# Kernel optimization log

Hardware: AMD Instinct MI355X
Metric: run time of the kernel (lower is better)

Reference implementation:

```python
import jax, jax.numpy as jnp
import numpy as np

EPS = 1e-5

def _layernorm(x, g, b):
    mu = jnp.mean(x, axis=-1, keepdims=True)
    var = jnp.mean(jnp.square(x - mu), axis=-1, keepdims=True)
    return (x - mu) * jax.lax.rsqrt(var + EPS) * g + b

def _time_shift(x):
    # xx[:, t] = x[:, t-1], xx[:, 0] = 0  (ZeroPad2d((0,0,1,-1)))
    return jnp.pad(x, ((0, 0), (1, 0), (0, 0)))[:, :-1, :]

def _wkv(time_decay, time_first, k, v):
    # Numerically-stable RWKV v4 recurrence (matches wkv_cuda forward).
    # k, v: [B, T, C]; time_decay, time_first: [C]
    w = -jnp.exp(time_decay)  # negative decay
    u = time_first
    B, T, C = k.shape
    aa0 = jnp.zeros((B, C), k.dtype)
    bb0 = jnp.zeros((B, C), k.dtype)
    pp0 = jnp.full((B, C), -1e38, k.dtype)

    def step(carry, kv_t):
        aa, bb, pp = carry
        kt, vt = kv_t
        ww = u + kt
        p = jnp.maximum(pp, ww)
        e1 = jnp.exp(pp - p)
        e2 = jnp.exp(ww - p)
        yt = (e1 * aa + e2 * vt) / (e1 * bb + e2)
        ww2 = pp + w
        p2 = jnp.maximum(ww2, kt)
        e1b = jnp.exp(ww2 - p2)
        e2b = jnp.exp(kt - p2)
        return (e1b * aa + e2b * vt, e1b * bb + e2b, p2), yt

    kT = jnp.swapaxes(k, 0, 1)  # [T, B, C]
    vT = jnp.swapaxes(v, 0, 1)
    _, y = jax.lax.scan(step, (aa0, bb0, pp0), (kT, vT))
    return jnp.swapaxes(y, 0, 1)  # [B, T, C]


def setup_inputs() -> dict:
    num_layers, layer_id, C = 8, 1, 512
    B, T = 512, 50
    H = 4 * C
    key = jax.random.key(0)
    ks = jax.random.split(key, 12)

    # parameter init mirroring the torch module's structured init
    ratio_0_to_1 = layer_id / (num_layers - 1)
    ratio_1_to_almost0 = 1.0 - layer_id / num_layers
    h = np.arange(C, dtype=np.float32)
    time_decay = (-5 + 8 * (h / (C - 1)) ** (0.7 + 1.3 * ratio_0_to_1)).astype(np.float32)
    zigzag = (np.array([(i + 1) % 3 - 1 for i in range(C)], dtype=np.float32)) * 0.5
    time_first = (np.ones(C, dtype=np.float32) * np.log(0.3) + zigzag).astype(np.float32)
    xr = (h / C).astype(np.float32)
    att_mix_k = (xr ** ratio_1_to_almost0)[None, None, :].astype(np.float32)
    att_mix_v = (xr ** ratio_1_to_almost0 + 0.3 * ratio_0_to_1)[None, None, :].astype(np.float32)
    att_mix_r = (xr ** (0.5 * ratio_1_to_almost0))[None, None, :].astype(np.float32)
    ffn_mix_k = att_mix_k.copy()
    ffn_mix_r = att_mix_k.copy()

    s = 0.02
    return {
        "x": jax.random.normal(ks[0], (B, T, C), jnp.float32),
        "ln1_g": jnp.ones((C,), jnp.float32), "ln1_b": jnp.zeros((C,), jnp.float32),
        "ln2_g": jnp.ones((C,), jnp.float32), "ln2_b": jnp.zeros((C,), jnp.float32),
        "att_mix_k": jnp.asarray(att_mix_k), "att_mix_v": jnp.asarray(att_mix_v),
        "att_mix_r": jnp.asarray(att_mix_r),
        "time_decay": jnp.asarray(time_decay), "time_first": jnp.asarray(time_first),
        "Wk": jax.random.normal(ks[1], (C, C), jnp.float32) * s,
        "Wv": jax.random.normal(ks[2], (C, C), jnp.float32) * s,
        "Wr": jax.random.normal(ks[3], (C, C), jnp.float32) * s,
        "Wo": jax.random.normal(ks[4], (C, C), jnp.float32) * s,
        "ffn_mix_k": jnp.asarray(ffn_mix_k), "ffn_mix_r": jnp.asarray(ffn_mix_r),
        "Fk": jax.random.normal(ks[5], (H, C), jnp.float32) * s,
        "Fv": jax.random.normal(ks[6], (C, H), jnp.float32) * s,
        "Fr": jax.random.normal(ks[7], (C, C), jnp.float32) * s,
    }


def reference(x, ln1_g, ln1_b, ln2_g, ln2_b,
              att_mix_k, att_mix_v, att_mix_r, time_decay, time_first,
              Wk, Wv, Wr, Wo, ffn_mix_k, ffn_mix_r, Fk, Fv, Fr):
    # --- time-mix (attention) branch ---
    h = _layernorm(x, ln1_g, ln1_b)
    hh = _time_shift(h)
    xk = h * att_mix_k + hh * (1 - att_mix_k)
    xv = h * att_mix_v + hh * (1 - att_mix_v)
    xr = h * att_mix_r + hh * (1 - att_mix_r)
    k = jnp.einsum('btc,dc->btd', xk, Wk)
    v = jnp.einsum('btc,dc->btd', xv, Wv)
    sr = jax.nn.sigmoid(jnp.einsum('btc,dc->btd', xr, Wr))
    rwkv = sr * _wkv(time_decay, time_first, k, v)
    x = x + jnp.einsum('btc,dc->btd', rwkv, Wo)

    # --- channel-mix (FFN) branch ---
    h = _layernorm(x, ln2_g, ln2_b)
    hh = _time_shift(h)
    fk = h * ffn_mix_k + hh * (1 - ffn_mix_k)
    fr = h * ffn_mix_r + hh * (1 - ffn_mix_r)
    kk = jnp.einsum('btc,hc->bth', fk, Fk)
    kk = jnp.square(jax.nn.relu(kk))
    kv = jnp.einsum('bth,ch->btc', kk, Fv)
    rkv = jax.nn.sigmoid(jnp.einsum('btc,dc->btd', fr, Fr)) * kv
    return x + rkv
```

## Files before the change

### kernel.cpp

```cpp
#include <hip/hip_runtime.h>
#include <stdint.h>

typedef unsigned short u16;
typedef __bf16 bf16x8 __attribute__((ext_vector_type(8)));
typedef float f32x4 __attribute__((ext_vector_type(4)));

#define DEV static __device__ __forceinline__

DEV u16 f2b(float f) {
    unsigned u = __float_as_uint(f);
    u += 0x7FFF + ((u >> 16) & 1);
    return (u16)(u >> 16);
}
DEV float b2f(u16 h) { return __uint_as_float((unsigned)h << 16); }

DEV void load16(const void* g, void* l) {
    __builtin_amdgcn_global_load_lds((const __attribute__((address_space(1))) void*)g,
                                     (__attribute__((address_space(3))) void*)l, 16, 0, 0);
}

__global__ __launch_bounds__(256) void cvt_bf16(const float* __restrict__ src,
                                                u16* __restrict__ dst, int n) {
    int i = (blockIdx.x * 256 + threadIdx.x) * 4;
    if (i < n) {
        float4 f = *(const float4*)(src + i);
        ushort4 o;
        o.x = f2b(f.x); o.y = f2b(f.y); o.z = f2b(f.z); o.w = f2b(f.w);
        *(ushort4*)(dst + i) = o;
    }
}

template <int NOUT>
__global__ __launch_bounds__(256) void ln_mix(
    const float* __restrict__ x, const float* __restrict__ g, const float* __restrict__ be,
    const float* __restrict__ mk, const float* __restrict__ mv, const float* __restrict__ mr,
    u16* __restrict__ ok, u16* __restrict__ ov, u16* __restrict__ orr, int T) {
    const int C = 512;
    int row = blockIdx.x;
    int t = row % T;
    int tid = threadIdx.x;
    int c = tid * 2;
    const float* xt = x + (size_t)row * C;
    float2 vt = *(const float2*)(xt + c);
    float2 vp = make_float2(0.f, 0.f);
    if (t > 0) vp = *(const float2*)(xt - C + c);

    float s0 = vt.x + vt.y, s1 = vt.x * vt.x + vt.y * vt.y;
    float s2 = vp.x + vp.y, s3 = vp.x * vp.x + vp.y * vp.y;
#pragma unroll
    for (int off = 32; off; off >>= 1) {
        s0 += __shfl_down(s0, off); s1 += __shfl_down(s1, off);
        s2 += __shfl_down(s2, off); s3 += __shfl_down(s3, off);
    }
    __shared__ float sm[16];
    int w = tid >> 6;
    if ((tid & 63) == 0) { sm[w*4+0] = s0; sm[w*4+1] = s1; sm[w*4+2] = s2; sm[w*4+3] = s3; }
    __syncthreads();
    s0 = sm[0] + sm[4] + sm[8]  + sm[12];
    s1 = sm[1] + sm[5] + sm[9]  + sm[13];
    s2 = sm[2] + sm[6] + sm[10] + sm[14];
    s3 = sm[3] + sm[7] + sm[11] + sm[15];

    const float rC = 1.f / 512.f;
    float mu_t = s0 * rC, var_t = s1 * rC - mu_t * mu_t;
    float mu_p = s2 * rC, var_p = s3 * rC - mu_p * mu_p;
    float rs_t = rsqrtf(var_t + 1e-5f);
    float rs_p = rsqrtf(var_p + 1e-5f);

    float xk0[2], xv0[2], xr0[2];
#pragma unroll
    for (int j = 0; j < 2; ++j) {
        int cc = c + j;
        float gg = g[cc], bb = be[cc];
        float xv_ = (j ? vt.y : vt.x);
        float xp_ = (j ? vp.y : vp.x);
        float h  = (xv_ - mu_t) * rs_t * gg + bb;
        float hh = (t > 0) ? ((xp_ - mu_p) * rs_p * gg + bb) : 0.f;
        float a = mk[cc];
        xk0[j] = h * a + hh * (1.f - a);
        if (NOUT == 3) { float av = mv[cc]; xv0[j] = h * av + hh * (1.f - av); }
        float ar = mr[cc];
        xr0[j] = h * ar + hh * (1.f - ar);
    }
    size_t idx = (size_t)row * C + c;
    *(ushort2*)&ok[idx] = make_ushort2(f2b(xk0[0]), f2b(xk0[1]));
    if (NOUT == 3) *(ushort2*)&ov[idx] = make_ushort2(f2b(xv0[0]), f2b(xv0[1]));
    *(ushort2*)&orr[idx] = make_ushort2(f2b(xr0[0]), f2b(xr0[1]));
}

template <int BN, int EPI>
__global__ __launch_bounds__(256) void gemm64(
    const u16* __restrict__ A0, int strideAz,
    const u16* __restrict__ B0, int strideBz,
    void* O0, void* O1, void* O2,
    const float* __restrict__ Add, const u16* __restrict__ Mul,
    int K, int D) {
    const int BM = 64, BK = 64;
    const int NT_ = BN / 32;
    __shared__ __align__(16) u16 As[BM * BK];
    __shared__ __align__(16) u16 Bs[BN * BK];

    int gx = gridDim.x, gy = gridDim.y;
    int fid = blockIdx.x + gx * (blockIdx.y + gy * blockIdx.z);
    int nwg = gx * gy * gridDim.z;
    int swz = (fid & 7) * (nwg >> 3) + (fid >> 3);
    int bx = swz % gx;
    int tmp = swz / gx;
    int by = tmp % gy;
    int bz = tmp / gy;

    const u16* A = A0 + (size_t)bz * strideAz;
    const u16* B = B0 + (size_t)bz * strideBz;
    void* Out = (bz == 0) ? O0 : (bz == 1) ? O1 : O2;

    int tid = threadIdx.x;
    int lane = tid & 63;
    int w = tid >> 6;
    int wm = w >> 1, wn = w & 1;
    int rowBase = by * BM;
    int colBase = bx * BN;
    int l8 = lane >> 3;
    int gsrc = ((lane & 7) ^ l8) * 8;

    f32x4 acc[2][NT_] = {};

    for (int kt = 0; kt < K; kt += BK) {
#pragma unroll
        for (int i = 0; i < 2; ++i) {
            int r0 = w * 16 + i * 8;
            load16(A + (size_t)(rowBase + r0 + l8) * K + kt + gsrc, &As[r0 * BK]);
        }
#pragma unroll
        for (int i = 0; i < BN / 32; ++i) {
            int r0 = w * (BN / 4) + i * 8;
            load16(B + (size_t)(colBase + r0 + l8) * K + kt + gsrc, &Bs[r0 * BK]);
        }
        __syncthreads();

        bf16x8 af[2][2], bfr[NT_][2];
#pragma unroll
        for (int m = 0; m < 2; ++m) {
            int row = wm * 32 + m * 16 + (lane & 15);
            int rx = row & 7;
#pragma unroll
            for (int s = 0; s < 2; ++s) {
                int gsw = (s * 4 + (lane >> 4)) ^ rx;
                af[m][s] = *(const bf16x8*)&As[row * BK + gsw * 8];
            }
        }
#pragma unroll
        for (int n = 0; n < NT_; ++n) {
            int col = wn * (BN / 2) + n * 16 + (lane & 15);
            int rx = col & 7;
#pragma unroll
            for (int s = 0; s < 2; ++s) {
                int gsw = (s * 4 + (lane >> 4)) ^ rx;
                bfr[n][s] = *(const bf16x8*)&Bs[col * BK + gsw * 8];
            }
        }
#pragma unroll
        for (int s = 0; s < 2; ++s)
#pragma unroll
            for (int m = 0; m < 2; ++m)
#pragma unroll
                for (int n = 0; n < NT_; ++n)
                    acc[m][n] = __builtin_amdgcn_mfma_f32_16x16x32_bf16(af[m][s], bfr[n][s], acc[m][n], 0, 0, 0);
        __syncthreads();
    }

    int r0e = (lane >> 4) * 4;
    int ce = lane & 15;
#pragma unroll
    for (int m = 0; m < 2; ++m) {
#pragma unroll
        for (int n = 0; n < NT_; ++n) {
            int row = rowBase + wm * 32 + m * 16 + r0e;
            int col = colBase + wn * (BN / 2) + n * 16 + ce;
#pragma unroll
            for (int r = 0; r < 4; ++r) {
                size_t idx = (size_t)(row + r) * D + col;
                float v = acc[m][n][r];
                if (EPI == 0) {
                    ((u16*)Out)[idx] = f2b(v);
                } else if (EPI == 2) {
                    ((float*)Out)[idx] = v + Add[idx];
                } else if (EPI == 3) {
                    float rr = fmaxf(v, 0.f);
                    ((u16*)Out)[idx] = f2b(rr * rr);
                } else if (EPI == 4) {
                    float s = 1.f / (1.f + __expf(-v));
                    ((float*)Out)[idx] = Add[idx] + s * b2f(Mul[idx]);
                } else {
                    ((u16*)Out)[idx] = (bz == 2) ? f2b(1.f / (1.f + __expf(-v))) : f2b(v);
                }
            }
        }
    }
}

__global__ __launch_bounds__(256) void wkv_kernel(
    const u16* __restrict__ k, const u16* __restrict__ v, const u16* __restrict__ sr,
    const float* __restrict__ td, const float* __restrict__ tf,
    u16* __restrict__ rwkv, int T) {
    const int C = 512;
    int gid = blockIdx.x * 256 + threadIdx.x;
    int c = gid & (C - 1);
    int b = gid >> 9;
    float w = -__expf(td[c]);
    float u = tf[c];
    float aa = 0.f, bb = 0.f, pp = -1e38f;
    size_t idx = (size_t)b * T * C + c;
    for (int t = 0; t < T; ++t, idx += C) {
        float kt = b2f(k[idx]), vt = b2f(v[idx]);
        float ww = u + kt;
        float p = fmaxf(pp, ww);
        float e1 = __expf(pp - p), e2 = __expf(ww - p);
        float y = (e1 * aa + e2 * vt) / (e1 * bb + e2);
        float ww2 = pp + w;
        float p2 = fmaxf(ww2, kt);
        float e1b = __expf(ww2 - p2), e2b = __expf(kt - p2);
        aa = e1b * aa + e2b * vt;
        bb = e1b * bb + e2b;
        pp = p2;
        rwkv[idx] = f2b(b2f(sr[idx]) * y);
    }
}

extern "C" void kernel_launch(void* const* d_in, const int* in_sizes, int n_in,
                              void* d_out, int out_size, void* d_ws, size_t ws_size,
                              hipStream_t stream) {
    const int B = 512, T = 50, C = 512, H = 2048;
    const int NT = B * T;

    const float* x     = (const float*)d_in[0];
    const float* ln1_g = (const float*)d_in[1];
    const float* ln1_b = (const float*)d_in[2];
    const float* ln2_g = (const float*)d_in[3];
    const float* ln2_b = (const float*)d_in[4];
    const float* amk   = (const float*)d_in[5];
    const float* amv   = (const float*)d_in[6];
    const float* amr   = (const float*)d_in[7];
    const float* td    = (const float*)d_in[8];
    const float* tf    = (const float*)d_in[9];
    const float* Wk    = (const float*)d_in[10];
    const float* Wv    = (const float*)d_in[11];
    const float* Wr    = (const float*)d_in[12];
    const float* Wo    = (const float*)d_in[13];
    const float* fmk   = (const float*)d_in[14];
    const float* fmr   = (const float*)d_in[15];
    const float* Fk    = (const float*)d_in[16];
    const float* Fv    = (const float*)d_in[17];
    const float* Fr    = (const float*)d_in[18];
    float* out = (float*)d_out;

    const size_t WBYTES = ((size_t)C*C*2)*6 + ((size_t)H*C*2)*2 + 4096;
    int R = 6400;
    if (ws_size >= (size_t)25600 * 1024 * 7 + WBYTES)      R = 25600;
    else if (ws_size >= (size_t)12800 * 1024 * 7 + WBYTES) R = 12800;
    const int NCH = NT / R;

    char* ws = (char*)d_ws;
    size_t off = 0;
    auto alloc = [&](size_t bytes) {
        char* p = ws + off;
        off += (bytes + 255) & ~(size_t)255;
        return p;
    };
    const size_t uc = (size_t)R * C * 2;
    u16*   U0 = (u16*)alloc(uc);
    u16*   U1 = (u16*)alloc(uc);
    u16*   U2 = (u16*)alloc(uc);
    u16*   U3 = (u16*)alloc(uc);
    u16*   U4 = (u16*)alloc(uc);
    float* X2 = (float*)alloc((size_t)R * C * 4);
    u16*   U5 = (u16*)X2;
    u16* bWkvr = (u16*)alloc((size_t)3 * C * C * 2);
    u16* bWo   = (u16*)alloc((size_t)C * C * 2);
    u16* bFk   = (u16*)alloc((size_t)H * C * 2);
    u16* bFv   = (u16*)alloc((size_t)C * H * 2);
    u16* bFr   = (u16*)alloc((size_t)C * C * 2);
    u16* kk = U0;

    cvt_bf16<<<C * C / 1024, 256, 0, stream>>>(Wk, bWkvr,             C * C);
    cvt_bf16<<<C * C / 1024, 256, 0, stream>>>(Wv, bWkvr + C * C,     C * C);
    cvt_bf16<<<C * C / 1024, 256, 0, stream>>>(Wr, bWkvr + 2 * C * C, C * C);
    cvt_bf16<<<C * C / 1024, 256, 0, stream>>>(Wo, bWo, C * C);
    cvt_bf16<<<H * C / 1024, 256, 0, stream>>>(Fk, bFk, H * C);
    cvt_bf16<<<C * H / 1024, 256, 0, stream>>>(Fv, bFv, C * H);
    cvt_bf16<<<C * C / 1024, 256, 0, stream>>>(Fr, bFr, C * C);

    for (int ch = 0; ch < NCH; ++ch) {
        const float* xc  = x   + (size_t)ch * R * C;
        float*       oc  = out + (size_t)ch * R * C;

        ln_mix<3><<<R, 256, 0, stream>>>(xc, ln1_g, ln1_b, amk, amv, amr, U0, U1, U2, T);
        gemm64<128, 5><<<dim3(C / 128, R / 64, 3), 256, 0, stream>>>(
            U0, R * C, bWkvr, C * C, U3, U4, U5, nullptr, nullptr, C, C);
        wkv_kernel<<<(R / T) * C / 256, 256, 0, stream>>>(U3, U4, U5, td, tf, U0, T);
        gemm64<128, 2><<<dim3(C / 128, R / 64, 1), 256, 0, stream>>>(
            U0, 0, bWo, 0, X2, nullptr, nullptr, xc, nullptr, C, C);

        ln_mix<2><<<R, 256, 0, stream>>>(X2, ln2_g, ln2_b, fmk, nullptr, fmr, U3, nullptr, U4, T);
        for (int hh = 0; hh < 2; ++hh) {
            size_t ro = (size_t)hh * (R / 2);
            gemm64<128, 3><<<dim3(H / 128, R / 128, 1), 256, 0, stream>>>(
                U3 + ro * C, 0, bFk, 0, kk, nullptr, nullptr, nullptr, nullptr, C, H);
            gemm64<64, 0><<<dim3(C / 64, R / 128, 1), 256, 0, stream>>>(
                kk, 0, bFv, 0, U2 + ro * C, nullptr, nullptr, nullptr, nullptr, H, C);
        }
        gemm64<128, 4><<<dim3(C / 128, R / 64, 1), 256, 0, stream>>>(
            U4, 0, bFr, 0, oc, nullptr, nullptr, X2, U2, C, C);
    }
}
```

Measured before the change: 540.9 us.

## Switch to double-buffered 128x128 GEMM tiles, sequential LayerNorm, single weight conversion

The 64-row GEMM is replaced by a 128x128 tile GEMM that double-buffers its LDS stages, so the next K-slice loads while MFMAs run. It also adds an XCD swizzle that handles workgroup counts not divisible by eight. LayerNorm+mix now runs one block per sequence and walks time steps, reusing the previous normalized row instead of recomputing it. The seven weight-conversion launches become one. Larger tiles and the per-sequence LN cut grid parallelism: the LN kernel drops to R/T blocks with a serial loop over T. The doubled LDS footprint may also lower occupancy.

```diff
diff --git a/kernel.cpp b/kernel.cpp
--- a/kernel.cpp
+++ b/kernel.cpp
@@ -19,91 +19,90 @@
                                      (__attribute__((address_space(3))) void*)l, 16, 0, 0);
 }
 
-__global__ __launch_bounds__(256) void cvt_bf16(const float* __restrict__ src,
-                                                u16* __restrict__ dst, int n) {
-    int i = (blockIdx.x * 256 + threadIdx.x) * 4;
-    if (i < n) {
-        float4 f = *(const float4*)(src + i);
-        ushort4 o;
-        o.x = f2b(f.x); o.y = f2b(f.y); o.z = f2b(f.z); o.w = f2b(f.w);
-        *(ushort4*)(dst + i) = o;
-    }
+__global__ __launch_bounds__(256) void cvt_all(
+    const float* __restrict__ Wk, const float* __restrict__ Wv,
+    const float* __restrict__ Wr, const float* __restrict__ Wo,
+    const float* __restrict__ Fk, const float* __restrict__ Fv,
+    const float* __restrict__ Fr, u16* __restrict__ dst) {
+    const int CC = 512 * 512, HC = 2048 * 512;
+    int e = (blockIdx.x * 256 + threadIdx.x) * 4;
+    const float* s; int base;
+    if      (e < 1 * CC)      { s = Wk; base = 0; }
+    else if (e < 2 * CC)      { s = Wv; base = 1 * CC; }
+    else if (e < 3 * CC)      { s = Wr; base = 2 * CC; }
+    else if (e < 4 * CC)      { s = Wo; base = 3 * CC; }
+    else if (e < 4 * CC + HC) { s = Fk; base = 4 * CC; }
+    else if (e < 4 * CC + 2 * HC) { s = Fv; base = 4 * CC + HC; }
+    else                      { s = Fr; base = 4 * CC + 2 * HC; }
+    float4 f = *(const float4*)(s + (e - base));
+    ushort4 o;
+    o.x = f2b(f.x); o.y = f2b(f.y); o.z = f2b(f.z); o.w = f2b(f.w);
+    *(ushort4*)(dst + e) = o;
 }
 
 template <int NOUT>
-__global__ __launch_bounds__(256) void ln_mix(
+__global__ __launch_bounds__(256) void ln_seq(
     const float* __restrict__ x, const float* __restrict__ g, const float* __restrict__ be,
     const float* __restrict__ mk, const float* __restrict__ mv, const float* __restrict__ mr,
     u16* __restrict__ ok, u16* __restrict__ ov, u16* __restrict__ orr, int T) {
     const int C = 512;
-    int row = blockIdx.x;
-    int t = row % T;
+    int b = blockIdx.x;
     int tid = threadIdx.x;
     int c = tid * 2;
-    const float* xt = x + (size_t)row * C;
-    float2 vt = *(const float2*)(xt + c);
-    float2 vp = make_float2(0.f, 0.f);
-    if (t > 0) vp = *(const float2*)(xt - C + c);
-
-    float s0 = vt.x + vt.y, s1 = vt.x * vt.x + vt.y * vt.y;
-    float s2 = vp.x + vp.y, s3 = vp.x * vp.x + vp.y * vp.y;
-#pragma unroll
-    for (int off = 32; off; off >>= 1) {
-        s0 += __shfl_down(s0, off); s1 += __shfl_down(s1, off);
-        s2 += __shfl_down(s2, off); s3 += __shfl_down(s3, off);
-    }
-    __shared__ float sm[16];
-    int w = tid >> 6;
-    if ((tid & 63) == 0) { sm[w*4+0] = s0; sm[w*4+1] = s1; sm[w*4+2] = s2; sm[w*4+3] = s3; }
-    __syncthreads();
-    s0 = sm[0] + sm[4] + sm[8]  + sm[12];
-    s1 = sm[1] + sm[5] + sm[9]  + sm[13];
-    s2 = sm[2] + sm[6] + sm[10] + sm[14];
-    s3 = sm[3] + sm[7] + sm[11] + sm[15];
-
-    const float rC = 1.f / 512.f;
-    float mu_t = s0 * rC, var_t = s1 * rC - mu_t * mu_t;
-    float mu_p = s2 * rC, var_p = s3 * rC - mu_p * mu_p;
-    float rs_t = rsqrtf(var_t + 1e-5f);
-    float rs_p = rsqrtf(var_p + 1e-5f);
-
-    float xk0[2], xv0[2], xr0[2];
-#pragma unroll
-    for (int j = 0; j < 2; ++j) {
-        int cc = c + j;
-        float gg = g[cc], bb = be[cc];
-        float xv_ = (j ? vt.y : vt.x);
-        float xp_ = (j ? vp.y : vp.x);
-        float h  = (xv_ - mu_t) * rs_t * gg + bb;
-        float hh = (t > 0) ? ((xp_ - mu_p) * rs_p * gg + bb) : 0.f;
-        float a = mk[cc];
-        xk0[j] = h * a + hh * (1.f - a);
-        if (NOUT == 3) { float av = mv[cc]; xv0[j] = h * av + hh * (1.f - av); }
-        float ar = mr[cc];
-        xr0[j] = h * ar + hh * (1.f - ar);
-    }
-    size_t idx = (size_t)row * C + c;
-    *(ushort2*)&ok[idx] = make_ushort2(f2b(xk0[0]), f2b(xk0[1]));
-    if (NOUT == 3) *(ushort2*)&ov[idx] = make_ushort2(f2b(xv0[0]), f2b(xv0[1]));
-    *(ushort2*)&orr[idx] = make_ushort2(f2b(xr0[0]), f2b(xr0[1]));
-}
-
-template <int BN, int EPI>
-__global__ __launch_bounds__(256) void gemm64(
+    const float* xb = x + (size_t)b * T * C;
+    float g0 = g[c], g1 = g[c + 1], be0 = be[c], be1 = be[c + 1];
+    float k0 = mk[c], k1 = mk[c + 1];
+    float v0 = 0.f, v1 = 0.f;
+    if (NOUT == 3) { v0 = mv[c]; v1 = mv[c + 1]; }
+    float r0 = mr[c], r1 = mr[c + 1];
+    __shared__ float sm[2][8];
+    float h0p = 0.f, h1p = 0.f;
+    size_t idx = (size_t)b * T * C + c;
+    for (int t = 0; t < T; ++t) {
+        float2 vt = *(const float2*)(xb + (size_t)t * C + c);
+        float s0 = vt.x + vt.y, s1 = vt.x * vt.x + vt.y * vt.y;
+#pragma unroll
+        for (int off = 32; off; off >>= 1) {
+            s0 += __shfl_down(s0, off); s1 += __shfl_down(s1, off);
+        }
+        int w = tid >> 6;
+        if ((tid & 63) == 0) { sm[t & 1][w * 2] = s0; sm[t & 1][w * 2 + 1] = s1; }
+        __syncthreads();
+        s0 = sm[t & 1][0] + sm[t & 1][2] + sm[t & 1][4] + sm[t & 1][6];
+        s1 = sm[t & 1][1] + sm[t & 1][3] + sm[t & 1][5] + sm[t & 1][7];
+        float mu = s0 * (1.f / 512.f);
+        float var = s1 * (1.f / 512.f) - mu * mu;
+        float rs = rsqrtf(var + 1e-5f);
+        float h0 = (vt.x - mu) * rs * g0 + be0;
+        float h1 = (vt.y - mu) * rs * g1 + be1;
+        *(ushort2*)&ok[idx] = make_ushort2(f2b(h0 * k0 + h0p * (1.f - k0)),
+                                           f2b(h1 * k1 + h1p * (1.f - k1)));
+        if (NOUT == 3)
+            *(ushort2*)&ov[idx] = make_ushort2(f2b(h0 * v0 + h0p * (1.f - v0)),
+                                               f2b(h1 * v1 + h1p * (1.f - v1)));
+        *(ushort2*)&orr[idx] = make_ushort2(f2b(h0 * r0 + h0p * (1.f - r0)),
+                                            f2b(h1 * r1 + h1p * (1.f - r1)));
+        h0p = h0; h1p = h1;
+        idx += C;
+    }
+}
+
+template <int EPI>
+__global__ __launch_bounds__(256) void gemm128(
     const u16* __restrict__ A0, int strideAz,
     const u16* __restrict__ B0, int strideBz,
     void* O0, void* O1, void* O2,
     const float* __restrict__ Add, const u16* __restrict__ Mul,
     int K, int D) {
-    const int BM = 64, BK = 64;
-    const int NT_ = BN / 32;
-    __shared__ __align__(16) u16 As[BM * BK];
-    __shared__ __align__(16) u16 Bs[BN * BK];
+    const int BM = 128, BN = 128, BK = 64;
+    __shared__ __align__(16) u16 As[2][BM * BK];
+    __shared__ __align__(16) u16 Bs[2][BN * BK];
 
     int gx = gridDim.x, gy = gridDim.y;
     int fid = blockIdx.x + gx * (blockIdx.y + gy * blockIdx.z);
     int nwg = gx * gy * gridDim.z;
-    int swz = (fid & 7) * (nwg >> 3) + (fid >> 3);
+    int q = nwg >> 3, r = nwg & 7, xcd = fid & 7, jj = fid >> 3;
+    int swz = (xcd < r ? xcd * (q + 1) : r * (q + 1) + (xcd - r) * q) + jj;
     int bx = swz % gx;
     int tmp = swz / gx;
     int by = tmp % gy;
@@ -113,80 +112,73 @@
     const u16* B = B0 + (size_t)bz * strideBz;
     void* Out = (bz == 0) ? O0 : (bz == 1) ? O1 : O2;
 
-    int tid = threadIdx.x;
-    int lane = tid & 63;
-    int w = tid >> 6;
+    int tid = threadIdx.x, lane = tid & 63, w = tid >> 6;
     int wm = w >> 1, wn = w & 1;
-    int rowBase = by * BM;
-    int colBase = bx * BN;
+    int rowBase = by * BM, colBase = bx * BN;
     int l8 = lane >> 3;
     int gsrc = ((lane & 7) ^ l8) * 8;
 
-    f32x4 acc[2][NT_] = {};
-
-    for (int kt = 0; kt < K; kt += BK) {
-#pragma unroll
-        for (int i = 0; i < 2; ++i) {
-            int r0 = w * 16 + i * 8;
-            load16(A + (size_t)(rowBase + r0 + l8) * K + kt + gsrc, &As[r0 * BK]);
-        }
-#pragma unroll
-        for (int i = 0; i < BN / 32; ++i) {
-            int r0 = w * (BN / 4) + i * 8;
-            load16(B + (size_t)(colBase + r0 + l8) * K + kt + gsrc, &Bs[r0 * BK]);
+    const int nt = K / BK;
+    f32x4 acc[4][4] = {};
+
+    auto stage = [&](int buf, int kt) {
+#pragma unroll
+        for (int i = 0; i < 4; ++i) {
+            int rr0 = w * 32 + i * 8;
+            load16(A + (size_t)(rowBase + rr0 + l8) * K + kt + gsrc, &As[buf][rr0 * BK]);
+            load16(B + (size_t)(colBase + rr0 + l8) * K + kt + gsrc, &Bs[buf][rr0 * BK]);
+        }
+    };
+
+    stage(0, 0);
+    __syncthreads();
+    int cur = 0;
+    for (int t = 0; t < nt; ++t) {
+        if (t + 1 < nt) stage(cur ^ 1, (t + 1) * BK);
+#pragma unroll
+        for (int s = 0; s < 2; ++s) {
+            bf16x8 af[4], bfv[4];
+#pragma unroll
+            for (int m = 0; m < 4; ++m) {
+                int row = wm * 64 + m * 16 + (lane & 15);
+                int gsw = (s * 4 + (lane >> 4)) ^ (row & 7);
+                af[m] = *(const bf16x8*)&As[cur][row * BK + gsw * 8];
+            }
+#pragma unroll
+            for (int n = 0; n < 4; ++n) {
+                int col = wn * 64 + n * 16 + (lane & 15);
+                int gsw = (s * 4 + (lane >> 4)) ^ (col & 7);
+                bfv[n] = *(const bf16x8*)&Bs[cur][col * BK + gsw * 8];
+            }
+#pragma unroll
+            for (int m = 0; m < 4; ++m)
+#pragma unroll
+                for (int n = 0; n < 4; ++n)
+                    acc[m][n] = __builtin_amdgcn_mfma_f32_16x16x32_bf16(af[m], bfv[n], acc[m][n], 0, 0, 0);
         }
         __syncthreads();
-
-        bf16x8 af[2][2], bfr[NT_][2];
-#pragma unroll
-        for (int m = 0; m < 2; ++m) {
-            int row = wm * 32 + m * 16 + (lane & 15);
-            int rx = row & 7;
-#pragma unroll
-            for (int s = 0; s < 2; ++s) {
-                int gsw = (s * 4 + (lane >> 4)) ^ rx;
-                af[m][s] = *(const bf16x8*)&As[row * BK + gsw * 8];
-            }
-        }
-#pragma unroll
-        for (int n = 0; n < NT_; ++n) {
-            int col = wn * (BN / 2) + n * 16 + (lane & 15);
-            int rx = col & 7;
-#pragma unroll
-            for (int s = 0; s < 2; ++s) {
-                int gsw = (s * 4 + (lane >> 4)) ^ rx;
-                bfr[n][s] = *(const bf16x8*)&Bs[col * BK + gsw * 8];
-            }
-        }
-#pragma unroll
-        for (int s = 0; s < 2; ++s)
-#pragma unroll
-            for (int m = 0; m < 2; ++m)
-#pragma unroll
-                for (int n = 0; n < NT_; ++n)
-                    acc[m][n] = __builtin_amdgcn_mfma_f32_16x16x32_bf16(af[m][s], bfr[n][s], acc[m][n], 0, 0, 0);
-        __syncthreads();
+        cur ^= 1;
     }
 
     int r0e = (lane >> 4) * 4;
     int ce = lane & 15;
 #pragma unroll
-    for (int m = 0; m < 2; ++m) {
-#pragma unroll
-        for (int n = 0; n < NT_; ++n) {
-            int row = rowBase + wm * 32 + m * 16 + r0e;
-            int col = colBase + wn * (BN / 2) + n * 16 + ce;
-#pragma unroll
-            for (int r = 0; r < 4; ++r) {
-                size_t idx = (size_t)(row + r) * D + col;
-                float v = acc[m][n][r];
+    for (int m = 0; m < 4; ++m) {
+#pragma unroll
+        for (int n = 0; n < 4; ++n) {
+            int row = rowBase + wm * 64 + m * 16 + r0e;
+            int col = colBase + wn * 64 + n * 16 + ce;
+#pragma unroll
+            for (int rr = 0; rr < 4; ++rr) {
+                size_t idx = (size_t)(row + rr) * D + col;
+                float v = acc[m][n][rr];
                 if (EPI == 0) {
                     ((u16*)Out)[idx] = f2b(v);
                 } else if (EPI == 2) {
                     ((float*)Out)[idx] = v + Add[idx];
                 } else if (EPI == 3) {
-                    float rr = fmaxf(v, 0.f);
-                    ((u16*)Out)[idx] = f2b(rr * rr);
+                    float rl = fmaxf(v, 0.f);
+                    ((u16*)Out)[idx] = f2b(rl * rl);
                 } else if (EPI == 4) {
                     float s = 1.f / (1.f + __expf(-v));
                     ((float*)Out)[idx] = Add[idx] + s * b2f(Mul[idx]);
@@ -281,34 +273,29 @@
     u16* bFr   = (u16*)alloc((size_t)C * C * 2);
     u16* kk = U0;
 
-    cvt_bf16<<<C * C / 1024, 256, 0, stream>>>(Wk, bWkvr,             C * C);
-    cvt_bf16<<<C * C / 1024, 256, 0, stream>>>(Wv, bWkvr + C * C,     C * C);
-    cvt_bf16<<<C * C / 1024, 256, 0, stream>>>(Wr, bWkvr + 2 * C * C, C * C);
-    cvt_bf16<<<C * C / 1024, 256, 0, stream>>>(Wo, bWo, C * C);
-    cvt_bf16<<<H * C / 1024, 256, 0, stream>>>(Fk, bFk, H * C);
-    cvt_bf16<<<C * H / 1024, 256, 0, stream>>>(Fv, bFv, C * H);
-    cvt_bf16<<<C * C / 1024, 256, 0, stream>>>(Fr, bFr, C * C);
+    cvt_all<<<(5 * C * C + 2 * H * C) / 1024, 256, 0, stream>>>(
+        Wk, Wv, Wr, Wo, Fk, Fv, Fr, bWkvr);
 
     for (int ch = 0; ch < NCH; ++ch) {
         const float* xc  = x   + (size_t)ch * R * C;
         float*       oc  = out + (size_t)ch * R * C;
 
-        ln_mix<3><<<R, 256, 0, stream>>>(xc, ln1_g, ln1_b, amk, amv, amr, U0, U1, U2, T);
-        gemm64<128, 5><<<dim3(C / 128, R / 64, 3), 256, 0, stream>>>(
+        ln_seq<3><<<R / T, 256, 0, stream>>>(xc, ln1_g, ln1_b, amk, amv, amr, U0, U1, U2, T);
+        gemm128<5><<<dim3(C / 128, R / 128, 3), 256, 0, stream>>>(
             U0, R * C, bWkvr, C * C, U3, U4, U5, nullptr, nullptr, C, C);
         wkv_kernel<<<(R / T) * C / 256, 256, 0, stream>>>(U3, U4, U5, td, tf, U0, T);
-        gemm64<128, 2><<<dim3(C / 128, R / 64, 1), 256, 0, stream>>>(
+        gemm128<2><<<dim3(C / 128, R / 128, 1), 256, 0, stream>>>(
             U0, 0, bWo, 0, X2, nullptr, nullptr, xc, nullptr, C, C);
 
-        ln_mix<2><<<R, 256, 0, stream>>>(X2, ln2_g, ln2_b, fmk, nullptr, fmr, U3, nullptr, U4, T);
+        ln_seq<2><<<R / T, 256, 0, stream>>>(X2, ln2_g, ln2_b, fmk, nullptr, fmr, U3, nullptr, U4, T);
         for (int hh = 0; hh < 2; ++hh) {
             size_t ro = (size_t)hh * (R / 2);
-            gemm64<128, 3><<<dim3(H / 128, R / 128, 1), 256, 0, stream>>>(
+            gemm128<3><<<dim3(H / 128, R / 256, 1), 256, 0, stream>>>(
                 U3 + ro * C, 0, bFk, 0, kk, nullptr, nullptr, nullptr, nullptr, C, H);
-            gemm64<64, 0><<<dim3(C / 64, R / 128, 1), 256, 0, stream>>>(
+            gemm128<0><<<dim3(C / 128, R / 256, 1), 256, 0, stream>>>(
                 kk, 0, bFv, 0, U2 + ro * C, nullptr, nullptr, nullptr, nullptr, H, C);
         }
-        gemm64<128, 4><<<dim3(C / 128, R / 64, 1), 256, 0, stream>>>(
+        gemm128<4><<<dim3(C / 128, R / 128, 1), 256, 0, stream>>>(
             U4, 0, bFr, 0, oc, nullptr, nullptr, X2, U2, C, C);
     }
 }
```

Result: slower. 579.6 us (+7.2%).
